# Kernel optimization log

Hardware: AMD Instinct MI355X
Metric: run time of the kernel (lower is better)

Reference implementation:

```python
import jax, jax.numpy as jnp
import numpy as np

LN_EPS = 1e-5

def _layernorm(x, g, b):
    mu = jnp.mean(x, axis=-1, keepdims=True)
    var = jnp.mean(jnp.square(x - mu), axis=-1, keepdims=True)
    return (x - mu) * jax.lax.rsqrt(var + LN_EPS) * g + b

def setup_inputs() -> dict:
    key = jax.random.key(0)
    B, T, C = 8, 2048, 1024
    ks = jax.random.split(key, 16)
    s = 1.0 / np.sqrt(C)
    inp = {
        'x':   jax.random.normal(ks[0], (B, T, C), dtype=jnp.float32),
        'Wq':  jax.random.uniform(ks[1], (C, C), jnp.float32, -s, s),
        'bq':  jax.random.uniform(ks[2], (C,), jnp.float32, -s, s),
        'Wk':  jax.random.uniform(ks[3], (C, C), jnp.float32, -s, s),
        'bk':  jax.random.uniform(ks[4], (C,), jnp.float32, -s, s),
        'Wv':  jax.random.uniform(ks[5], (C, C), jnp.float32, -s, s),
        'bv':  jax.random.uniform(ks[6], (C,), jnp.float32, -s, s),
        'g1':  jnp.ones((C,), jnp.float32),
        'be1': jnp.zeros((C,), jnp.float32),
        'W1':  jax.random.uniform(ks[7], (C, C), jnp.float32, -s, s),
        'bf1': jax.random.uniform(ks[8], (C,), jnp.float32, -s, s),
        'W2':  jax.random.uniform(ks[9], (C, C), jnp.float32, -s, s),
        'bf2': jax.random.uniform(ks[10], (C,), jnp.float32, -s, s),
        'g2':  jnp.ones((C,), jnp.float32),
        'be2': jnp.zeros((C,), jnp.float32),
    }
    return inp

def reference(x, Wq, bq, Wk, bk, Wv, bv, g1, be1, W1, bf1, W2, bf2, g2, be2):
    B, T, C = x.shape
    q = x @ Wq + bq
    k = x @ Wk + bk
    v = x @ Wv + bv
    # FFT cross-correlation along time axis
    fq = jnp.fft.rfft(q, axis=1)
    fk = jnp.fft.rfft(k, axis=1)
    corr = jnp.fft.irfft(fq * jnp.conj(fk), n=T, axis=1)  # [B,T,C]
    weights = jax.nn.softmax(corr, axis=1)
    # einsum 'btd,btv->btd': weights * sum over v's channel dim
    attn = weights * jnp.sum(v, axis=-1, keepdims=True)
    x = _layernorm(x + attn, g1, be1)
    h = jax.nn.relu(x @ W1 + bf1) @ W2 + bf2
    x = _layernorm(x + h, g2, be2)
    return x
```

## Files before the change

### kernel.cpp

```cpp
#include <hip/hip_runtime.h>
#include <math.h>

#define B_DIM 8
#define T_DIM 2048
#define C_DIM 1024
#define BT_DIM (B_DIM * T_DIM)
#define FSZ ((size_t)BT_DIM * C_DIM)
#define LN_EPS 1e-5f

typedef __bf16 bf16x8 __attribute__((ext_vector_type(8)));
typedef _Float16 f16x8 __attribute__((ext_vector_type(8)));
typedef float f32x4 __attribute__((ext_vector_type(4)));

__device__ __forceinline__ unsigned short f2bf(float f) {
  __bf16 h = (__bf16)f;
  return __builtin_bit_cast(unsigned short, h);
}
__device__ __forceinline__ unsigned short f2h(float f) {
  _Float16 h = (_Float16)f;
  return __builtin_bit_cast(unsigned short, h);
}

__device__ __forceinline__ void gld16(const void* g, void* l) {
  __builtin_amdgcn_global_load_lds(
      (const __attribute__((address_space(1))) unsigned int*)g,
      (__attribute__((address_space(3))) unsigned int*)l, 16, 0, 0);
}

__device__ __forceinline__ int swz(int a) {
  return a ^ (((a >> 4) ^ (a >> 8)) & 15);
}

__device__ __forceinline__ int enc11(int f) {
  return ((f & 3) << 9) | (((f >> 2) & 3) << 7) | (((f >> 4) & 3) << 5) |
         (((f >> 6) & 3) << 3) | (((f >> 8) & 3) << 1) | ((f >> 10) & 1);
}

__global__ __launch_bounds__(256)
void cvt_split_sv_kernel(const float* __restrict__ x, const float* __restrict__ wvsum,
                         const float* __restrict__ bvsum,
                         unsigned short* __restrict__ hi, unsigned short* __restrict__ lo,
                         float* __restrict__ sv) {
  const int r = blockIdx.x;
  const int tid = threadIdx.x;
  const size_t base = (size_t)r * C_DIM + (tid << 2);
  float4 v = *(const float4*)(x + base);
  float4 w = *(const float4*)(wvsum + (tid << 2));
  float f[4] = {v.x, v.y, v.z, v.w};
  unsigned short hv[4], lv[4];
#pragma unroll
  for (int i = 0; i < 4; i++) {
    _Float16 hb = (_Float16)f[i];
    hv[i] = __builtin_bit_cast(unsigned short, hb);
    lv[i] = f2h(f[i] - (float)hb);
  }
  *(ushort4*)(hi + base) = make_ushort4(hv[0], hv[1], hv[2], hv[3]);
  *(ushort4*)(lo + base) = make_ushort4(lv[0], lv[1], lv[2], lv[3]);
  float s = v.x * w.x + v.y * w.y + v.z * w.z + v.w * w.w;
#pragma unroll
  for (int off = 32; off > 0; off >>= 1) s += __shfl_down(s, off);
  __shared__ float ps[4];
  if ((tid & 63) == 0) ps[tid >> 6] = s;
  __syncthreads();
  if (tid == 0) sv[r] = ps[0] + ps[1] + ps[2] + ps[3] + bvsum[0];
}

__global__ __launch_bounds__(256)
void wtrans_f16_kernel(const float* __restrict__ W, unsigned short* __restrict__ Wt,
                       int K, int N) {
  __shared__ float tile[32][33];
  const int tid = threadIdx.x;
  const int tx = tid & 31, ty = tid >> 5;
  const int n0 = blockIdx.x * 32, k0 = blockIdx.y * 32;
#pragma unroll
  for (int i = 0; i < 4; i++) {
    int row = ty + i * 8;
    tile[row][tx] = W[(size_t)(k0 + row) * N + n0 + tx];
  }
  __syncthreads();
#pragma unroll
  for (int i = 0; i < 4; i++) {
    int row = ty + i * 8;
    Wt[(size_t)(n0 + row) * K + k0 + tx] = f2h(tile[tx][row]);
  }
}

__global__ __launch_bounds__(256)
void wtrans_kernel(const float* __restrict__ W, unsigned short* __restrict__ Wt,
                   int K, int N) {
  __shared__ float tile[32][33];
  const int tid = threadIdx.x;
  const int tx = tid & 31, ty = tid >> 5;
  const int n0 = blockIdx.x * 32, k0 = blockIdx.y * 32;
#pragma unroll
  for (int i = 0; i < 4; i++) {
    int row = ty + i * 8;
    tile[row][tx] = W[(size_t)(k0 + row) * N + n0 + tx];
  }
  __syncthreads();
#pragma unroll
  for (int i = 0; i < 4; i++) {
    int row = ty + i * 8;
    Wt[(size_t)(n0 + row) * K + k0 + tx] = f2bf(tile[tx][row]);
  }
}

__global__ __launch_bounds__(256)
void wv_rowsum_kernel(const float* __restrict__ Wv, const float* __restrict__ bv,
                      float* __restrict__ wvsum, float* __restrict__ bvsum) {
  const int r = blockIdx.x;
  const int tid = threadIdx.x;
  const float* src = (r < C_DIM) ? (Wv + (size_t)r * C_DIM) : bv;
  float4 t4 = *(const float4*)(src + (tid << 2));
  float s = t4.x + t4.y + t4.z + t4.w;
#pragma unroll
  for (int off = 32; off > 0; off >>= 1) s += __shfl_down(s, off);
  __shared__ float ps[4];
  if ((tid & 63) == 0) ps[tid >> 6] = s;
  __syncthreads();
  if (tid == 0) {
    float v = ps[0] + ps[1] + ps[2] + ps[3];
    if (r < C_DIM) wvsum[r] = v; else bvsum[0] = v;
  }
}

__global__ __launch_bounds__(256, 2)
void gemm_bf16_kernel(const __bf16* __restrict__ A, const __bf16* __restrict__ Bt,
                      const float* __restrict__ bias, float* Yf, unsigned short* Yb,
                      int K, int N, int do_relu) {
  __shared__ __align__(16) __bf16 As[128 * 32];
  __shared__ __align__(16) __bf16 Bs[128 * 32];
  const int tid = threadIdx.x;
  const int wave = tid >> 6, lane = tid & 63;
  const int wr = wave >> 1, wc = wave & 1;
  const int r15 = lane & 15, kq = lane >> 4;
  const int h = blockIdx.y * 8 + blockIdx.x;
  const int xcd = h & 7, s = h >> 3;
  const int mIdx = (xcd << 4) + (s & 7) + ((s >> 6) << 3);
  const int nIdx = (s >> 3) & 7;
  const int m0 = mIdx * 128, n0 = nIdx * 128;

  f32x4 acc[4][4] = {};

  for (int k0 = 0; k0 < K; k0 += 32) {
#pragma unroll
    for (int r = 0; r < 2; ++r) {
      int idx = r * 256 + tid;
      int row = idx >> 2;
      int ko = (idx & 3) ^ ((row >> 1) & 3);
      gld16(A + (size_t)(m0 + row) * K + k0 + ko * 8, &As[idx * 8]);
      gld16(Bt + (size_t)(n0 + row) * K + k0 + ko * 8, &Bs[idx * 8]);
    }
    __syncthreads();
    bf16x8 afr[4], bfr[4];
#pragma unroll
    for (int i = 0; i < 4; i++) {
      int ar = wr * 64 + i * 16 + r15;
      afr[i] = *(const bf16x8*)&As[(ar * 4 + (kq ^ ((ar >> 1) & 3))) * 8];
      int br = wc * 64 + i * 16 + r15;
      bfr[i] = *(const bf16x8*)&Bs[(br * 4 + (kq ^ ((br >> 1) & 3))) * 8];
    }
#pragma unroll
    for (int mi = 0; mi < 4; mi++)
#pragma unroll
      for (int ni = 0; ni < 4; ni++)
        acc[mi][ni] = __builtin_amdgcn_mfma_f32_16x16x32_bf16(afr[mi], bfr[ni], acc[mi][ni], 0, 0, 0);
    __syncthreads();
  }

  float bv[4];
#pragma unroll
  for (int ni = 0; ni < 4; ni++) bv[ni] = bias[n0 + wc * 64 + ni * 16 + r15];

#pragma unroll
  for (int mi = 0; mi < 4; mi++)
#pragma unroll
    for (int ni = 0; ni < 4; ni++) {
      const int n = n0 + wc * 64 + ni * 16 + r15;
#pragma unroll
      for (int r = 0; r < 4; r++) {
        const int m = m0 + wr * 64 + mi * 16 + kq * 4 + r;
        float v = acc[mi][ni][r] + bv[ni];
        if (do_relu) v = fmaxf(v, 0.f);
        if (Yf) Yf[(size_t)m * N + n] = v;
        if (Yb) Yb[(size_t)m * N + n] = f2bf(v);
      }
    }
}

__global__ __launch_bounds__(512, 2)
void gemm_qkT_f16_8ph_kernel(const _Float16* __restrict__ Ahi, const _Float16* __restrict__ Alo,
                             const _Float16* __restrict__ Bq, const _Float16* __restrict__ Bk,
                             const float* __restrict__ biasq, const float* __restrict__ biask,
                             float* __restrict__ Yq, float* __restrict__ Yk, int K, int N) {
  __shared__ __align__(16) _Float16 AhL[3][256 * 32];
  __shared__ __align__(16) _Float16 AlL[3][256 * 32];
  __shared__ __align__(16) _Float16 BqL[3][128 * 32];
  __shared__ __align__(16) _Float16 BkL[3][128 * 32];

  const int tid = threadIdx.x;
  const int wave = tid >> 6, lane = tid & 63;
  const int wr = wave >> 2, wc = wave & 3;
  const int r15 = lane & 15, kq = lane >> 4;
  const int h = blockIdx.y * 8 + blockIdx.x;
  const int xcd = h & 7, s = h >> 3;
  const int mIdx = (xcd << 3) + (s & 3) + ((s >> 5) << 2);
  const int nIdx = (s >> 2) & 7;
  const int m0 = mIdx * 256, n0 = nIdx * 128;
  const int NT = K >> 5;

  const int row_a0 = tid >> 2;
  const int row_a1 = row_a0 + 128;
  const int ch = tid & 3;
  const int ko0 = ch ^ ((row_a0 >> 1) & 3);
  const int ko1 = ch ^ ((row_a1 >> 1) & 3);
  const _Float16* agh0 = Ahi + (size_t)(m0 + row_a0) * K + ko0 * 8;
  const _Float16* agl0 = Alo + (size_t)(m0 + row_a0) * K + ko0 * 8;
  const _Float16* agh1 = Ahi + (size_t)(m0 + row_a1) * K + ko1 * 8;
  const _Float16* agl1 = Alo + (size_t)(m0 + row_a1) * K + ko1 * 8;
  const _Float16* bgq  = Bq  + (size_t)(n0 + row_a0) * K + ko0 * 8;
  const _Float16* bgk  = Bk  + (size_t)(n0 + row_a0) * K + ko0 * 8;

  const int ksel = kq ^ ((r15 >> 1) & 3);
  const int aoff = (wr * 128 + r15) * 32 + ksel * 8;
  const int boff = (wc * 32 + r15) * 32 + ksel * 8;

  f32x4 accq[8][2] = {};
  f32x4 acck[8][2] = {};

  gld16(agh0 + 0, &AhL[0][(size_t)tid * 8]);
  gld16(agl0 + 0, &AlL[0][(size_t)tid * 8]);
  gld16(agh1 + 0, &AhL[0][(size_t)(tid + 512) * 8]);
  gld16(agl1 + 0, &AlL[0][(size_t)(tid + 512) * 8]);
  gld16(bgq + 0, &BqL[0][(size_t)tid * 8]);
  gld16(bgk + 0, &BkL[0][(size_t)tid * 8]);
  gld16(agh0 + 32, &AhL[1][(size_t)tid * 8]);
  gld16(agl0 + 32, &AlL[1][(size_t)tid * 8]);
  gld16(agh1 + 32, &AhL[1][(size_t)(tid + 512) * 8]);
  gld16(agl1 + 32, &AlL[1][(size_t)(tid + 512) * 8]);
  gld16(bgq + 32, &BqL[1][(size_t)tid * 8]);
  gld16(bgk + 32, &BkL[1][(size_t)tid * 8]);

  int bR = 0;
  int bS = 2;

  for (int j = 0; j < NT; ++j) {
    if (j < NT - 1) {
      asm volatile("s_waitcnt vmcnt(6)" ::: "memory");
    } else {
      asm volatile("s_waitcnt vmcnt(0)" ::: "memory");
    }
    __builtin_amdgcn_s_barrier();
    __builtin_amdgcn_sched_barrier(0);

    const int kk = (j + 2) * 32;
    const bool doStage = (j + 2 < NT);

    f16x8 bqf[2], bkf[2];
#pragma unroll
    for (int ni = 0; ni < 2; ++ni) {
      bqf[ni] = *(const f16x8*)&BqL[bR][boff + ni * 512];
      bkf[ni] = *(const f16x8*)&BkL[bR][boff + ni * 512];
    }

#pragma unroll
    for (int p = 0; p < 4; ++p) {
      f16x8 ah0 = *(const f16x8*)&AhL[bR][aoff + (2 * p + 0) * 512];
      f16x8 al0 = *(const f16x8*)&AlL[bR][aoff + (2 * p + 0) * 512];
      f16x8 ah1 = *(const f16x8*)&AhL[bR][aoff + (2 * p + 1) * 512];
      f16x8 al1 = *(const f16x8*)&AlL[bR][aoff + (2 * p + 1) * 512];
      if (doStage) {
        if (p == 0) {
          gld16(agh0 + kk, &AhL[bS][(size_t)tid * 8]);
          gld16(agl0 + kk, &AlL[bS][(size_t)tid * 8]);
        }
        if (p == 1) {
          gld16(agh1 + kk, &AhL[bS][(size_t)(tid + 512) * 8]);
          gld16(agl1 + kk, &AlL[bS][(size_t)(tid + 512) * 8]);
        }
        if (p == 2) gld16(bgq + kk, &BqL[bS][(size_t)tid * 8]);
        if (p == 3) gld16(bgk + kk, &BkL[bS][(size_t)tid * 8]);
      }
      __builtin_amdgcn_s_barrier();
      asm volatile("s_waitcnt lgkmcnt(0)" ::: "memory");
      __builtin_amdgcn_sched_barrier(0);
      __builtin_amdgcn_s_setprio(1);
#pragma unroll
      for (int m2 = 0; m2 < 2; ++m2) {
        const int mi = 2 * p + m2;
        const f16x8 ahv = m2 ? ah1 : ah0;
        const f16x8 alv = m2 ? al1 : al0;
#pragma unroll
        for (int ni = 0; ni < 2; ++ni) {
          accq[mi][ni] = __builtin_amdgcn_mfma_f32_16x16x32_f16(ahv, bqf[ni], accq[mi][ni], 0, 0, 0);
          accq[mi][ni] = __builtin_amdgcn_mfma_f32_16x16x32_f16(alv, bqf[ni], accq[mi][ni], 0, 0, 0);
          acck[mi][ni] = __builtin_amdgcn_mfma_f32_16x16x32_f16(ahv, bkf[ni], acck[mi][ni], 0, 0, 0);
          acck[mi][ni] = __builtin_amdgcn_mfma_f32_16x16x32_f16(alv, bkf[ni], acck[mi][ni], 0, 0, 0);
        }
      }
      __builtin_amdgcn_s_setprio(0);
      __builtin_amdgcn_sched_barrier(0);
    }

    bR = (bR + 1 == 3) ? 0 : bR + 1;
    bS = (bS + 1 == 3) ? 0 : bS + 1;
  }

  float bvq[2], bvk[2];
#pragma unroll
  for (int ni = 0; ni < 2; ++ni) {
    bvq[ni] = biasq[n0 + wc * 32 + ni * 16 + r15];
    bvk[ni] = biask[n0 + wc * 32 + ni * 16 + r15];
  }

#pragma unroll
  for (int mi = 0; mi < 8; ++mi) {
    const int mbase = m0 + wr * 128 + mi * 16 + kq * 4;
    const int bb = mbase >> 11;
    const int t = mbase & (T_DIM - 1);
#pragma unroll
    for (int ni = 0; ni < 2; ++ni) {
      const int n = n0 + wc * 32 + ni * 16 + r15;
      const size_t o = ((size_t)bb * C_DIM + n) * T_DIM + t;
      *(float4*)(Yq + o) = make_float4(accq[mi][ni][0] + bvq[ni], accq[mi][ni][1] + bvq[ni],
                                       accq[mi][ni][2] + bvq[ni], accq[mi][ni][3] + bvq[ni]);
      *(float4*)(Yk + o) = make_float4(acck[mi][ni][0] + bvk[ni], acck[mi][ni][1] + bvk[ni],
                                       acck[mi][ni][2] + bvk[ni], acck[mi][ni][3] + bvk[ni]);
    }
  }
}

__device__ void fft_dif(float2* X, const float2* tw, int tid, float sgn) {
#pragma unroll
  for (int s = 0; s < 5; s++) {
    const int m = 512 >> (2 * s);
    const int jstep = 512 / m;
#pragma unroll
    for (int ii = 0; ii < 2; ii++) {
      const int i = tid + ii * 256;
      const int q = i & (m - 1);
      const int a0 = ((i - q) << 2) + q;
      float2 x0 = X[swz(a0)];
      float2 x1 = X[swz(a0 + m)];
      float2 x2 = X[swz(a0 + 2 * m)];
      float2 x3 = X[swz(a0 + 3 * m)];
      float2 t0 = make_float2(x0.x + x2.x, x0.y + x2.y);
      float2 t2 = make_float2(x0.x - x2.x, x0.y - x2.y);
      float2 t1 = make_float2(x1.x + x3.x, x1.y + x3.y);
      float2 t3 = make_float2(x1.x - x3.x, x1.y - x3.y);
      const float jx = -sgn * t3.y, jy = sgn * t3.x;
      float2 y0 = make_float2(t0.x + t1.x, t0.y + t1.y);
      float2 y1 = make_float2(t2.x + jx, t2.y + jy);
      float2 y2 = make_float2(t0.x - t1.x, t0.y - t1.y);
      float2 y3 = make_float2(t2.x - jx, t2.y - jy);
      const int j1 = q * jstep;
      float2 tv = tw[swz(j1)];
      const float c1 = tv.x, s1 = tv.y * sgn;
      const float c2 = c1 * c1 - s1 * s1, s2 = 2.f * c1 * s1;
      const float c3 = c2 * c1 - s2 * s1, s3 = c2 * s1 + s2 * c1;
      X[swz(a0)] = y0;
      X[swz(a0 + m)] = make_float2(c1 * y1.x - s1 * y1.y, c1 * y1.y + s1 * y1.x);
      X[swz(a0 + 2 * m)] = make_float2(c2 * y2.x - s2 * y2.y, c2 * y2.y + s2 * y2.x);
      X[swz(a0 + 3 * m)] = make_float2(c3 * y3.x - s3 * y3.y, c3 * y3.y + s3 * y3.x);
    }
    __syncthreads();
  }
#pragma unroll
  for (int ii = 0; ii < 4; ii++) {
    const int a = (tid + ii * 256) << 1;
    float2 u = X[swz(a)], v = X[swz(a + 1)];
    X[swz(a)] = make_float2(u.x + v.x, u.y + v.y);
    X[swz(a + 1)] = make_float2(u.x - v.x, u.y - v.y);
  }
  __syncthreads();
}

__device__ void fft_dit_inv(float2* X, const float2* tw, int tid) {
#pragma unroll
  for (int ii = 0; ii < 4; ii++) {
    const int a = (tid + ii * 256) << 1;
    float2 u = X[swz(a)], v = X[swz(a + 1)];
    X[swz(a)] = make_float2(u.x + v.x, u.y + v.y);
    X[swz(a + 1)] = make_float2(u.x - v.x, u.y - v.y);
  }
  __syncthreads();
#pragma unroll
  for (int s = 4; s >= 0; s--) {
    const int m = 512 >> (2 * s);
    const int jstep = 512 / m;
#pragma unroll
    for (int ii = 0; ii < 2; ii++) {
      const int i = tid + ii * 256;
      const int q = i & (m - 1);
      const int a0 = ((i - q) << 2) + q;
      float2 v0 = X[swz(a0)];
      float2 v1 = X[swz(a0 + m)];
      float2 v2 = X[swz(a0 + 2 * m)];
      float2 v3 = X[swz(a0 + 3 * m)];
      const int j1 = q * jstep;
      float2 tv = tw[swz(j1)];
      const float c1 = tv.x, s1 = tv.y;
      const float c2 = c1 * c1 - s1 * s1, s2 = 2.f * c1 * s1;
      const float c3 = c2 * c1 - s2 * s1, s3 = c2 * s1 + s2 * c1;
      float2 w1 = make_float2(c1 * v1.x - s1 * v1.y, c1 * v1.y + s1 * v1.x);
      float2 w2 = make_float2(c2 * v2.x - s2 * v2.y, c2 * v2.y + s2 * v2.x);
      float2 w3 = make_float2(c3 * v3.x - s3 * v3.y, c3 * v3.y + s3 * v3.x);
      float2 t0 = make_float2(v0.x + w2.x, v0.y + w2.y);
      float2 t2 = make_float2(v0.x - w2.x, v0.y - w2.y);
      float2 t1 = make_float2(w1.x + w3.x, w1.y + w3.y);
      float2 t3 = make_float2(w1.x - w3.x, w1.y - w3.y);
      const float jx = -t3.y, jy = t3.x;
      X[swz(a0)] = make_float2(t0.x + t1.x, t0.y + t1.y);
      X[swz(a0 + m)] = make_float2(t2.x + jx, t2.y + jy);
      X[swz(a0 + 2 * m)] = make_float2(t0.x - t1.x, t0.y - t1.y);
      X[swz(a0 + 3 * m)] = make_float2(t2.x - jx, t2.y - jy);
    }
    __syncthreads();
  }
}

__global__ __launch_bounds__(256)
void corr_fft_kernel(const float* qT, const float* kT, float* corrT,
                     float* __restrict__ Mv, float* __restrict__ Iv) {
  __shared__ float2 bA[2048];
  __shared__ float2 bB[2048];
  __shared__ float2 tw[512];
  __shared__ float2 red[4];
  const int tid = threadIdx.x;
  const int wave = tid >> 6, lane = tid & 63;
  const int b = blockIdx.y;
  const int c0 = blockIdx.x * 2;
  const float* q0 = qT + ((size_t)b * C_DIM + c0) * T_DIM;
  const float* k0p = kT + ((size_t)b * C_DIM + c0) * T_DIM;

#pragma unroll
  for (int jj = 0; jj < 2; jj++) {
    int j = tid + jj * 256;
    float sA, cA;
    __sincosf((float)j * (6.283185307179586f / 2048.0f), &sA, &cA);
    tw[swz(j)] = make_float2(cA, sA);
  }

#pragma unroll
  for (int jj = 0; jj < 8; jj++) {
    int t = tid + jj * 256;
    bA[swz(t)] = make_float2(q0[t], q0[t + T_DIM]);
    bB[swz(t)] = make_float2(k0p[t], k0p[t + T_DIM]);
  }
  __syncthreads();

  fft_dif(bA, tw, tid, -1.0f);
  fft_dif(bB, tw, tid, -1.0f);

#pragma unroll 1
  for (int f = tid; f <= 1024; f += 256) {
    const int g = (2048 - f) & 2047;
    const int p = swz(enc11(f));
    const int p2 = swz(enc11(g));
    float2 Zq = bA[p], Zq2 = bA[p2];
    float2 Zk = bB[p], Zk2 = bB[p2];
    float2 Aq = make_float2(0.5f * (Zq.x + Zq2.x), 0.5f * (Zq.y - Zq2.y));
    float2 Dq = make_float2(Zq.x - Zq2.x, Zq.y + Zq2.y);
    float2 Bq = make_float2(0.5f * Dq.y, -0.5f * Dq.x);
    float2 Ak = make_float2(0.5f * (Zk.x + Zk2.x), 0.5f * (Zk.y - Zk2.y));
    float2 Dk = make_float2(Zk.x - Zk2.x, Zk.y + Zk2.y);
    float2 Bk = make_float2(0.5f * Dk.y, -0.5f * Dk.x);
    float2 G = make_float2(Aq.x * Ak.x + Aq.y * Ak.y, Aq.y * Ak.x - Aq.x * Ak.y);
    float2 H = make_float2(Bq.x * Bk.x + Bq.y * Bk.y, Bq.y * Bk.x - Bq.x * Bk.y);
    bA[p] = make_float2(G.x - H.y, G.y + H.x);
    if (p2 != p) bA[p2] = make_float2(G.x + H.y, -G.y + H.x);
  }
  __syncthreads();

  fft_dit_inv(bA, tw, tid);

  float* o0 = corrT + ((size_t)b * C_DIM + c0) * T_DIM;
  const float sc = 1.0f / 2048.0f;
  float mx0 = -INFINITY, mx1 = -INFINITY;
#pragma unroll
  for (int jj = 0; jj < 8; jj++) {
    int t = tid + jj * 256;
    float2 o = bA[swz(t)];
    float v0 = o.x * sc, v1 = o.y * sc;
    o0[t] = v0;
    o0[t + T_DIM] = v1;
    mx0 = fmaxf(mx0, v0);
    mx1 = fmaxf(mx1, v1);
  }
#pragma unroll
  for (int off = 32; off > 0; off >>= 1) {
    mx0 = fmaxf(mx0, __shfl_down(mx0, off));
    mx1 = fmaxf(mx1, __shfl_down(mx1, off));
  }
  if (lane == 0) red[wave] = make_float2(mx0, mx1);
  __syncthreads();
  const float M0 = fmaxf(fmaxf(red[0].x, red[1].x), fmaxf(red[2].x, red[3].x));
  const float M1 = fmaxf(fmaxf(red[0].y, red[1].y), fmaxf(red[2].y, red[3].y));
  __syncthreads();
  float s0 = 0.f, s1 = 0.f;
#pragma unroll
  for (int jj = 0; jj < 8; jj++) {
    int t = tid + jj * 256;
    float2 o = bA[swz(t)];
    s0 += __expf(o.x * sc - M0);
    s1 += __expf(o.y * sc - M1);
  }
#pragma unroll
  for (int off = 32; off > 0; off >>= 1) {
    s0 += __shfl_down(s0, off);
    s1 += __shfl_down(s1, off);
  }
  if (lane == 0) red[wave] = make_float2(s0, s1);
  __syncthreads();
  if (tid == 0) {
    float S0 = red[0].x + red[1].x + red[2].x + red[3].x;
    float S1 = red[0].y + red[1].y + red[2].y + red[3].y;
    Mv[(size_t)b * C_DIM + c0] = M0;
    Mv[(size_t)b * C_DIM + c0 + 1] = M1;
    Iv[(size_t)b * C_DIM + c0] = 1.0f / S0;
    Iv[(size_t)b * C_DIM + c0 + 1] = 1.0f / S1;
  }
}

__global__ __launch_bounds__(512)
void attn_ln_kernel(const float* __restrict__ corrT, const float* __restrict__ Mv,
                    const float* __restrict__ Iv, const float* __restrict__ sv,
                    const float* __restrict__ x, const float* __restrict__ g,
                    const float* __restrict__ be, float* __restrict__ outf,
                    unsigned short* __restrict__ outb) {
  __shared__ float att[32][1028];
  const int tid = threadIdx.x;
  const int b = blockIdx.y;
  const int t0 = blockIdx.x * 32;

  const int tx = tid & 31;
  const int cy = tid >> 5;
  const float* cb = corrT + (size_t)b * C_DIM * T_DIM + t0 + tx;
  const float* Mb = Mv + (size_t)b * C_DIM;
  const float* Ib = Iv + (size_t)b * C_DIM;
#pragma unroll 8
  for (int it = 0; it < 64; ++it) {
    const int c = cy + (it << 4);
    float v = cb[(size_t)c * T_DIM];
    att[tx][c] = __expf(v - Mb[c]) * Ib[c];
  }
  __syncthreads();

  const int t = tid >> 4;
  const int l16 = tid & 15;
  const float svv = sv[(size_t)b * T_DIM + t0 + t];
  const float* xr = x + ((size_t)b * T_DIM + t0 + t) * C_DIM;
  float s = 0.f, s2 = 0.f;
#pragma unroll
  for (int j = 0; j < 16; ++j) {
    const int c = (l16 + (j << 4)) << 2;
    float4 xv = *(const float4*)(xr + c);
    float4 av = *(const float4*)&att[t][c];
    float v0 = xv.x + av.x * svv;
    float v1 = xv.y + av.y * svv;
    float v2 = xv.z + av.z * svv;
    float v3 = xv.w + av.w * svv;
    *(float4*)&att[t][c] = make_float4(v0, v1, v2, v3);
    s += v0 + v1 + v2 + v3;
    s2 += v0 * v0 + v1 * v1 + v2 * v2 + v3 * v3;
  }
#pragma unroll
  for (int off = 8; off > 0; off >>= 1) {
    s += __shfl_xor(s, off);
    s2 += __shfl_xor(s2, off);
  }
  const float mu = s * (1.0f / C_DIM);
  const float var = s2 * (1.0f / C_DIM) - mu * mu;
  const float rs = rsqrtf(var + LN_EPS);
  float* orow = outf + ((size_t)b * T_DIM + t0 + t) * C_DIM;
  unsigned short* obrow = outb + ((size_t)b * T_DIM + t0 + t) * C_DIM;
#pragma unroll
  for (int j = 0; j < 16; ++j) {
    const int c = (l16 + (j << 4)) << 2;
    float4 val = *(const float4*)&att[t][c];
    float4 gv = *(const float4*)(g + c);
    float4 bev = *(const float4*)(be + c);
    float o0 = (val.x - mu) * rs * gv.x + bev.x;
    float o1 = (val.y - mu) * rs * gv.y + bev.y;
    float o2 = (val.z - mu) * rs * gv.z + bev.z;
    float o3 = (val.w - mu) * rs * gv.w + bev.w;
    *(float4*)(orow + c) = make_float4(o0, o1, o2, o3);
    *(ushort4*)(obrow + c) = make_ushort4(f2bf(o0), f2bf(o1), f2bf(o2), f2bf(o3));
  }
}

__global__ __launch_bounds__(256)
void add_ln_kernel(const float* __restrict__ A, const float* __restrict__ Bv,
                   const float* __restrict__ g, const float* __restrict__ be,
                   float* __restrict__ outf, unsigned short* outb) {
  const int r = blockIdx.x;
  const int tid = threadIdx.x;
  const size_t base = (size_t)r * C_DIM + (tid << 2);
  float4 a = *(const float4*)(A + base);
  float4 b = *(const float4*)(Bv + base);
  float x0 = a.x + b.x, x1 = a.y + b.y, x2 = a.z + b.z, x3 = a.w + b.w;
  float s = x0 + x1 + x2 + x3;
  float s2 = x0 * x0 + x1 * x1 + x2 * x2 + x3 * x3;
#pragma unroll
  for (int off = 32; off > 0; off >>= 1) {
    s += __shfl_down(s, off);
    s2 += __shfl_down(s2, off);
  }
  __shared__ float ps[4], ps2[4];
  if ((tid & 63) == 0) { ps[tid >> 6] = s; ps2[tid >> 6] = s2; }
  __syncthreads();
  float S = ps[0] + ps[1] + ps[2] + ps[3];
  float S2 = ps2[0] + ps2[1] + ps2[2] + ps2[3];
  const float mu = S * (1.0f / C_DIM);
  const float var = S2 * (1.0f / C_DIM) - mu * mu;
  const float rs = rsqrtf(var + LN_EPS);
  float4 gv = *(const float4*)(g + (tid << 2));
  float4 bev = *(const float4*)(be + (tid << 2));
  float o0 = (x0 - mu) * rs * gv.x + bev.x;
  float o1 = (x1 - mu) * rs * gv.y + bev.y;
  float o2 = (x2 - mu) * rs * gv.z + bev.z;
  float o3 = (x3 - mu) * rs * gv.w + bev.w;
  *(float4*)(outf + base) = make_float4(o0, o1, o2, o3);
  if (outb) *(ushort4*)(outb + base) = make_ushort4(f2bf(o0), f2bf(o1), f2bf(o2), f2bf(o3));
}

extern "C" void kernel_launch(void* const* d_in, const int* in_sizes, int n_in,
                              void* d_out, int out_size, void* d_ws, size_t ws_size,
                              hipStream_t stream) {
  const float* x   = (const float*)d_in[0];
  const float* Wq  = (const float*)d_in[1];
  const float* bq  = (const float*)d_in[2];
  const float* Wk  = (const float*)d_in[3];
  const float* bk  = (const float*)d_in[4];
  const float* Wv  = (const float*)d_in[5];
  const float* bv  = (const float*)d_in[6];
  const float* g1  = (const float*)d_in[7];
  const float* be1 = (const float*)d_in[8];
  const float* W1  = (const float*)d_in[9];
  const float* bf1 = (const float*)d_in[10];
  const float* W2  = (const float*)d_in[11];
  const float* bf2 = (const float*)d_in[12];
  const float* g2  = (const float*)d_in[13];
  const float* be2 = (const float*)d_in[14];
  float* out = (float*)d_out;

  float* ws = (float*)d_ws;
  float* qbuf = ws;
  float* kbuf = ws + FSZ;
  unsigned short* xhi = (unsigned short*)(ws + 2 * FSZ);
  unsigned short* xlo = xhi + FSZ;
  unsigned short* wA = xlo + FSZ;
  unsigned short* wB = wA + (size_t)C_DIM * C_DIM;
  float* sv = (float*)(wB + (size_t)C_DIM * C_DIM);
  float* wvsum = sv + BT_DIM;
  float* bvsum = wvsum + C_DIM;
  float* Mv = bvsum + 1;
  float* Iv = Mv + (size_t)B_DIM * C_DIM;

  const dim3 blk(256);
  const dim3 ggrid(C_DIM / 128, BT_DIM / 128);
  const dim3 qkgrid(C_DIM / 128, BT_DIM / 256);
  const dim3 tgrid(C_DIM / 32, C_DIM / 32);

  wv_rowsum_kernel<<<dim3(C_DIM + 1), blk, 0, stream>>>(Wv, bv, wvsum, bvsum);

  cvt_split_sv_kernel<<<dim3(BT_DIM), blk, 0, stream>>>(x, wvsum, bvsum, xhi, xlo, sv);

  wtrans_f16_kernel<<<tgrid, blk, 0, stream>>>(Wq, wA, C_DIM, C_DIM);
  wtrans_f16_kernel<<<tgrid, blk, 0, stream>>>(Wk, wB, C_DIM, C_DIM);
  gemm_qkT_f16_8ph_kernel<<<qkgrid, dim3(512), 0, stream>>>(
      (const _Float16*)xhi, (const _Float16*)xlo,
      (const _Float16*)wA, (const _Float16*)wB,
      bq, bk, qbuf, kbuf, C_DIM, C_DIM);

  corr_fft_kernel<<<dim3(C_DIM / 2, B_DIM), blk, 0, stream>>>(qbuf, kbuf, qbuf, Mv, Iv);

  attn_ln_kernel<<<dim3(T_DIM / 32, B_DIM), dim3(512), 0, stream>>>(
      qbuf, Mv, Iv, sv, x, g1, be1, kbuf, xhi);

  wtrans_kernel<<<tgrid, blk, 0, stream>>>(W1, wA, C_DIM, C_DIM);
  wtrans_kernel<<<tgrid, blk, 0, stream>>>(W2, wB, C_DIM, C_DIM);

  gemm_bf16_kernel<<<ggrid, blk, 0, stream>>>((const __bf16*)xhi, (const __bf16*)wA,
                                              bf1, nullptr, xlo, C_DIM, C_DIM, 1);
  gemm_bf16_kernel<<<ggrid, blk, 0, stream>>>((const __bf16*)xlo, (const __bf16*)wB,
                                              bf2, qbuf, nullptr, C_DIM, C_DIM, 0);

  add_ln_kernel<<<dim3(BT_DIM), blk, 0, stream>>>(kbuf, qbuf, g2, be2, out, nullptr);
}
```

Baseline: 522.5 us.

## Store softmax exponentials in bf16 and drop fp32 LN1 output copy

The FFT correlation kernel now computes the exponentials itself and writes them as bf16 instead of fp32 raw correlations plus per-channel maxima, so the attention/LN kernel only loads bf16 values and multiplies by the inverse sum. The first layernorm no longer writes an fp32 copy; the final residual add reads the bf16 LN1 output instead. This cuts several full-tensor fp32 reads and writes across three kernels, at the cost of bf16 rounding in the softmax weights and in the residual path into the second layernorm.

```diff
diff --git a/kernel.cpp b/kernel.cpp
--- a/kernel.cpp
+++ b/kernel.cpp
@@ -19,6 +19,10 @@
 __device__ __forceinline__ unsigned short f2h(float f) {
   _Float16 h = (_Float16)f;
   return __builtin_bit_cast(unsigned short, h);
+}
+__device__ __forceinline__ float bf2f(unsigned short u) {
+  unsigned int v = ((unsigned int)u) << 16;
+  return __builtin_bit_cast(float, v);
 }
 
 __device__ __forceinline__ void gld16(const void* g, void* l) {
@@ -420,8 +424,8 @@
 }
 
 __global__ __launch_bounds__(256)
-void corr_fft_kernel(const float* qT, const float* kT, float* corrT,
-                     float* __restrict__ Mv, float* __restrict__ Iv) {
+void corr_fft_kernel(const float* qT, const float* kT, unsigned short* __restrict__ wT,
+                     float* __restrict__ Iv) {
   __shared__ float2 bA[2048];
   __shared__ float2 bB[2048];
   __shared__ float2 tw[512];
@@ -474,18 +478,15 @@
 
   fft_dit_inv(bA, tw, tid);
 
-  float* o0 = corrT + ((size_t)b * C_DIM + c0) * T_DIM;
+  unsigned short* o0 = wT + ((size_t)b * C_DIM + c0) * T_DIM;
   const float sc = 1.0f / 2048.0f;
   float mx0 = -INFINITY, mx1 = -INFINITY;
 #pragma unroll
   for (int jj = 0; jj < 8; jj++) {
     int t = tid + jj * 256;
     float2 o = bA[swz(t)];
-    float v0 = o.x * sc, v1 = o.y * sc;
-    o0[t] = v0;
-    o0[t + T_DIM] = v1;
-    mx0 = fmaxf(mx0, v0);
-    mx1 = fmaxf(mx1, v1);
+    mx0 = fmaxf(mx0, o.x);
+    mx1 = fmaxf(mx1, o.y);
   }
 #pragma unroll
   for (int off = 32; off > 0; off >>= 1) {
@@ -502,8 +503,12 @@
   for (int jj = 0; jj < 8; jj++) {
     int t = tid + jj * 256;
     float2 o = bA[swz(t)];
-    s0 += __expf(o.x * sc - M0);
-    s1 += __expf(o.y * sc - M1);
+    float e0 = __expf((o.x - M0) * sc);
+    float e1 = __expf((o.y - M1) * sc);
+    s0 += e0;
+    s1 += e1;
+    o0[t] = f2bf(e0);
+    o0[t + T_DIM] = f2bf(e1);
   }
 #pragma unroll
   for (int off = 32; off > 0; off >>= 1) {
@@ -515,18 +520,15 @@
   if (tid == 0) {
     float S0 = red[0].x + red[1].x + red[2].x + red[3].x;
     float S1 = red[0].y + red[1].y + red[2].y + red[3].y;
-    Mv[(size_t)b * C_DIM + c0] = M0;
-    Mv[(size_t)b * C_DIM + c0 + 1] = M1;
     Iv[(size_t)b * C_DIM + c0] = 1.0f / S0;
     Iv[(size_t)b * C_DIM + c0 + 1] = 1.0f / S1;
   }
 }
 
 __global__ __launch_bounds__(512)
-void attn_ln_kernel(const float* __restrict__ corrT, const float* __restrict__ Mv,
-                    const float* __restrict__ Iv, const float* __restrict__ sv,
-                    const float* __restrict__ x, const float* __restrict__ g,
-                    const float* __restrict__ be, float* __restrict__ outf,
+void attn_ln_kernel(const unsigned short* __restrict__ wT, const float* __restrict__ Iv,
+                    const float* __restrict__ sv, const float* __restrict__ x,
+                    const float* __restrict__ g, const float* __restrict__ be,
                     unsigned short* __restrict__ outb) {
   __shared__ float att[32][1028];
   const int tid = threadIdx.x;
@@ -535,14 +537,12 @@
 
   const int tx = tid & 31;
   const int cy = tid >> 5;
-  const float* cb = corrT + (size_t)b * C_DIM * T_DIM + t0 + tx;
-  const float* Mb = Mv + (size_t)b * C_DIM;
+  const unsigned short* cb = wT + (size_t)b * C_DIM * T_DIM + t0 + tx;
   const float* Ib = Iv + (size_t)b * C_DIM;
 #pragma unroll 8
   for (int it = 0; it < 64; ++it) {
     const int c = cy + (it << 4);
-    float v = cb[(size_t)c * T_DIM];
-    att[tx][c] = __expf(v - Mb[c]) * Ib[c];
+    att[tx][c] = bf2f(cb[(size_t)c * T_DIM]) * Ib[c];
   }
   __syncthreads();
 
@@ -572,7 +572,6 @@
   const float mu = s * (1.0f / C_DIM);
   const float var = s2 * (1.0f / C_DIM) - mu * mu;
   const float rs = rsqrtf(var + LN_EPS);
-  float* orow = outf + ((size_t)b * T_DIM + t0 + t) * C_DIM;
   unsigned short* obrow = outb + ((size_t)b * T_DIM + t0 + t) * C_DIM;
 #pragma unroll
   for (int j = 0; j < 16; ++j) {
@@ -584,21 +583,23 @@
     float o1 = (val.y - mu) * rs * gv.y + bev.y;
     float o2 = (val.z - mu) * rs * gv.z + bev.z;
     float o3 = (val.w - mu) * rs * gv.w + bev.w;
-    *(float4*)(orow + c) = make_float4(o0, o1, o2, o3);
     *(ushort4*)(obrow + c) = make_ushort4(f2bf(o0), f2bf(o1), f2bf(o2), f2bf(o3));
   }
 }
 
 __global__ __launch_bounds__(256)
-void add_ln_kernel(const float* __restrict__ A, const float* __restrict__ Bv,
-                   const float* __restrict__ g, const float* __restrict__ be,
-                   float* __restrict__ outf, unsigned short* outb) {
+void add_ln_bf_kernel(const unsigned short* __restrict__ A, const float* __restrict__ Bv,
+                      const float* __restrict__ g, const float* __restrict__ be,
+                      float* __restrict__ outf) {
   const int r = blockIdx.x;
   const int tid = threadIdx.x;
   const size_t base = (size_t)r * C_DIM + (tid << 2);
-  float4 a = *(const float4*)(A + base);
+  ushort4 a4 = *(const ushort4*)(A + base);
   float4 b = *(const float4*)(Bv + base);
-  float x0 = a.x + b.x, x1 = a.y + b.y, x2 = a.z + b.z, x3 = a.w + b.w;
+  float x0 = bf2f(a4.x) + b.x;
+  float x1 = bf2f(a4.y) + b.y;
+  float x2 = bf2f(a4.z) + b.z;
+  float x3 = bf2f(a4.w) + b.w;
   float s = x0 + x1 + x2 + x3;
   float s2 = x0 * x0 + x1 * x1 + x2 * x2 + x3 * x3;
 #pragma unroll
@@ -621,7 +622,6 @@
   float o2 = (x2 - mu) * rs * gv.z + bev.z;
   float o3 = (x3 - mu) * rs * gv.w + bev.w;
   *(float4*)(outf + base) = make_float4(o0, o1, o2, o3);
-  if (outb) *(ushort4*)(outb + base) = make_ushort4(f2bf(o0), f2bf(o1), f2bf(o2), f2bf(o3));
 }
 
 extern "C" void kernel_launch(void* const* d_in, const int* in_sizes, int n_in,
@@ -654,8 +654,7 @@
   float* sv = (float*)(wB + (size_t)C_DIM * C_DIM);
   float* wvsum = sv + BT_DIM;
   float* bvsum = wvsum + C_DIM;
-  float* Mv = bvsum + 1;
-  float* Iv = Mv + (size_t)B_DIM * C_DIM;
+  float* Iv = bvsum + 1;
 
   const dim3 blk(256);
   const dim3 ggrid(C_DIM / 128, BT_DIM / 128);
@@ -673,10 +672,10 @@
       (const _Float16*)wA, (const _Float16*)wB,
       bq, bk, qbuf, kbuf, C_DIM, C_DIM);
 
-  corr_fft_kernel<<<dim3(C_DIM / 2, B_DIM), blk, 0, stream>>>(qbuf, kbuf, qbuf, Mv, Iv);
+  corr_fft_kernel<<<dim3(C_DIM / 2, B_DIM), blk, 0, stream>>>(qbuf, kbuf, xlo, Iv);
 
   attn_ln_kernel<<<dim3(T_DIM / 32, B_DIM), dim3(512), 0, stream>>>(
-      qbuf, Mv, Iv, sv, x, g1, be1, kbuf, xhi);
+      xlo, Iv, sv, x, g1, be1, xhi);
 
   wtrans_kernel<<<tgrid, blk, 0, stream>>>(W1, wA, C_DIM, C_DIM);
   wtrans_kernel<<<tgrid, blk, 0, stream>>>(W2, wB, C_DIM, C_DIM);
@@ -686,5 +685,5 @@
   gemm_bf16_kernel<<<ggrid, blk, 0, stream>>>((const __bf16*)xlo, (const __bf16*)wB,
                                               bf2, qbuf, nullptr, C_DIM, C_DIM, 0);
 
-  add_ln_kernel<<<dim3(BT_DIM), blk, 0, stream>>>(kbuf, qbuf, g2, be2, out, nullptr);
-}
+  add_ln_bf_kernel<<<dim3(BT_DIM), blk, 0, stream>>>(xhi, qbuf, g2, be2, out);
+}
```

Measured after the change: 517.5 us. About the same (-1.0%).
